# Optimization experiments

Hardware: AMD Instinct MI355X
Metric: run time of the kernel (lower is better)

Reference implementation:

```python
import jax, jax.numpy as jnp
import numpy as np

D_MODEL, D_STATE, D_CONV, D_INNER = 1024, 16, 4, 2048
BATCH, SEQ = 2, 2048


def setup_inputs() -> dict:
    key = jax.random.key(0)
    ks = jax.random.split(key, 12)
    s = 0.02
    inp = {
        "x": jax.random.normal(ks[0], (BATCH, SEQ, D_MODEL), jnp.float32),
        # Linear weights stored (in, out): y = x @ W + b (equivalent to torch x @ W.T + b)
        "W_in": jax.random.normal(ks[1], (D_MODEL, 2 * D_INNER), jnp.float32) * s,
        "b_in": jnp.zeros((2 * D_INNER,), jnp.float32),
        # depthwise conv kernel (OIH) with groups=d_inner -> (d_inner, 1, d_conv)
        "conv_w": jax.random.normal(ks[2], (D_INNER, 1, D_CONV), jnp.float32) * s,
        "conv_b": jnp.zeros((D_INNER,), jnp.float32),
        "W_x": jax.random.normal(ks[3], (D_INNER, 2 * D_STATE), jnp.float32) * s,
        "b_x": jnp.zeros((2 * D_STATE,), jnp.float32),
        "W_dt": jax.random.normal(ks[4], (D_INNER, D_INNER), jnp.float32) * s,
        "b_dt": jnp.zeros((D_INNER,), jnp.float32),
        # A_log init: log(arange(1..d_state)) tiled over d_inner, as in the module
        "A_log": jnp.log(jnp.tile(jnp.arange(1, D_STATE + 1, dtype=jnp.float32), (D_INNER, 1))),
        "D": jnp.ones((D_INNER,), jnp.float32),
        "W_out": jax.random.normal(ks[5], (D_INNER, D_MODEL), jnp.float32) * s,
        "b_out": jnp.zeros((D_MODEL,), jnp.float32),
    }
    return inp


def reference(x, W_in, b_in, conv_w, conv_b, W_x, b_x, W_dt, b_dt, A_log, D, W_out, b_out):
    d_inner, d_state = A_log.shape
    d_conv = conv_w.shape[-1]
    bsz, seq_len, _ = x.shape

    xz = x @ W_in + b_in                      # (B, L, 2*Din)
    xh, z = jnp.split(xz, 2, axis=-1)

    # causal depthwise conv: torch pads both sides by d_conv-1 then slices [:L]
    # == left-pad-only causal conv
    xc = jnp.transpose(xh, (0, 2, 1))         # (B, Din, L)
    xc = jax.lax.conv_general_dilated(
        xc, conv_w, window_strides=(1,), padding=[(d_conv - 1, 0)],
        dimension_numbers=("NCH", "OIH", "NCH"), feature_group_count=d_inner)
    xc = xc + conv_b[None, :, None]
    xh = jax.nn.silu(jnp.transpose(xc, (0, 2, 1)))  # (B, L, Din)

    A = -jnp.exp(A_log)                       # (Din, N)
    x_dbl = xh @ W_x + b_x                    # (B, L, 2N)
    Bmat = x_dbl[..., d_state:]               # second chunk; first chunk is discarded
    delta = jax.nn.softplus(xh @ W_dt + b_dt) # (B, L, Din)

    def step(h, inp):
        d_t, b_t, u_t = inp                    # (B,Din), (B,N), (B,Din)
        dA = jnp.exp(d_t[:, :, None] * A)      # (B, Din, N)
        dBu = d_t[:, :, None] * b_t[:, None, :] * u_t[:, :, None]
        h = dA * h + dBu
        return h, h.sum(-1)                    # y_t: (B, Din)

    h0 = jnp.zeros((bsz, d_inner, d_state), x.dtype)
    _, ys = jax.lax.scan(step, h0, (jnp.swapaxes(delta, 0, 1),
                                    jnp.swapaxes(Bmat, 0, 1),
                                    jnp.swapaxes(xh, 0, 1)))
    y = jnp.swapaxes(ys, 0, 1) + xh * D       # skip connection with D
    y = y * jax.nn.silu(z)                    # gate
    return y @ W_out + b_out                  # (B, L, d_model)
```

## Files before the change

kernel.cpp:

```cpp
#include <hip/hip_runtime.h>
#include <stdint.h>

#define NDM   1024
#define NDS   16
#define NDC   4
#define NDI   2048
#define NB    2
#define NL    2048
#define MROWS (NB*NL)
#define CCH   32
#define CLEN  64

typedef __bf16 bf16x8 __attribute__((ext_vector_type(8)));
typedef float  f32x4  __attribute__((ext_vector_type(4)));
typedef short  short8 __attribute__((ext_vector_type(8)));

__device__ __forceinline__ short f2bf(float f) {
  union { float f; unsigned u; } x; x.f = f;
  unsigned r = (x.u + 0x7FFFu + ((x.u >> 16) & 1u)) >> 16;
  return (short)r;
}

__device__ __forceinline__ size_t fgoff(int row, int k8, int K) {
  return (size_t)(row >> 4) * K * 16 + (size_t)k8 * 128 + (row & 15) * 8;
}

__global__ __launch_bounds__(256) void cvt_fg_kernel(
    const float* __restrict__ in, short* __restrict__ out) {
  __shared__ short slab[16][1032];
  const int tid = threadIdx.x;
  const int g = blockIdx.x;
  const float* p = in + (size_t)g * 16 * 1024;
  #pragma unroll
  for (int u = 0; u < 8; ++u) {
    int unit = u * 256 + tid;
    int rr = unit >> 7, cc = unit & 127;
    const float* rp = p + (size_t)rr * 1024 + cc * 8;
    #pragma unroll
    for (int e = 0; e < 8; ++e) slab[rr][cc * 8 + e] = f2bf(rp[e]);
  }
  __syncthreads();
  short* op = out + (size_t)g * 16384;
  #pragma unroll
  for (int u = 0; u < 8; ++u) {
    int u2 = u * 256 + tid;
    int rr = u2 & 15, k8 = u2 >> 4;
    *(short8*)&op[k8 * 128 + rr * 8] = *(short8*)&slab[rr][k8 * 8];
  }
}

__global__ __launch_bounds__(256) void transpose_fg_kernel(
    const float* __restrict__ in, short* __restrict__ out, int K, int N) {
  __shared__ float t[64][33];
  const int tx = threadIdx.x, ty = threadIdx.y;
  const int n0 = blockIdx.x * 32, k0 = blockIdx.y * 64;
  #pragma unroll
  for (int i = 0; i < 64; i += 8)
    t[ty + i][tx] = in[(size_t)(k0 + ty + i) * N + n0 + tx];
  __syncthreads();
  const int n = n0 + tx, k8 = (k0 >> 3) + ty;
  short8 v;
  #pragma unroll
  for (int e = 0; e < 8; ++e) v[e] = f2bf(t[ty * 8 + e][tx]);
  *(short8*)&out[fgoff(n, k8, K)] = v;
}

template<int BN, int EPI>
__global__ __launch_bounds__(256, 2) void gemm_fg_kernel(
    const short* __restrict__ A, const short* __restrict__ Bt,
    const float* __restrict__ bias, float* __restrict__ C,
    int M, int N, int K)
{
  const int tid  = threadIdx.x;
  const int lane = tid & 63;
  const int w    = tid >> 6;
  const int wM   = w >> 1;
  const int wN   = w & 1;
  const int g    = lane >> 4;
  const int r    = lane & 15;

  constexpr int FN = BN / 32;

  const int nx  = gridDim.x;
  const int nwg = nx * gridDim.y;
  const int bid = blockIdx.y * nx + blockIdx.x;
  const int swz = (bid & 7) * (nwg >> 3) + (bid >> 3);
  const int bm  = (swz / nx) * 128;
  const int bn  = (swz % nx) * BN;

  const short* pA[4];
  const short* pB[FN];
  #pragma unroll
  for (int m = 0; m < 4; ++m)
    pA[m] = A + (size_t)((bm >> 4) + wM * 4 + m) * K * 16 + lane * 8;
  #pragma unroll
  for (int n = 0; n < FN; ++n)
    pB[n] = Bt + (size_t)((bn >> 4) + wN * FN + n) * K * 16 + lane * 8;

  f32x4 acc[4][FN];
  #pragma unroll
  for (int m = 0; m < 4; ++m)
    #pragma unroll
    for (int n = 0; n < FN; ++n)
      acc[m][n] = (f32x4){0.f, 0.f, 0.f, 0.f};

  bf16x8 a0[4], b0[FN], a1[4], b1[FN];
  #pragma unroll
  for (int m = 0; m < 4; ++m) a0[m] = *(const bf16x8*)(pA[m]);
  #pragma unroll
  for (int n = 0; n < FN; ++n) b0[n] = *(const bf16x8*)(pB[n]);

  for (int kb = 0; kb < K; kb += 64) {
    if (kb + 32 < K) {
      #pragma unroll
      for (int m = 0; m < 4; ++m)
        a1[m] = *(const bf16x8*)(pA[m] + (size_t)(kb + 32) * 16);
      #pragma unroll
      for (int n = 0; n < FN; ++n)
        b1[n] = *(const bf16x8*)(pB[n] + (size_t)(kb + 32) * 16);
    }
    #pragma unroll
    for (int m = 0; m < 4; ++m)
      #pragma unroll
      for (int n = 0; n < FN; ++n)
        acc[m][n] = __builtin_amdgcn_mfma_f32_16x16x32_bf16(
            a0[m], b0[n], acc[m][n], 0, 0, 0);

    if (kb + 64 < K) {
      #pragma unroll
      for (int m = 0; m < 4; ++m)
        a0[m] = *(const bf16x8*)(pA[m] + (size_t)(kb + 64) * 16);
      #pragma unroll
      for (int n = 0; n < FN; ++n)
        b0[n] = *(const bf16x8*)(pB[n] + (size_t)(kb + 64) * 16);
    }
    #pragma unroll
    for (int m = 0; m < 4; ++m)
      #pragma unroll
      for (int n = 0; n < FN; ++n)
        acc[m][n] = __builtin_amdgcn_mfma_f32_16x16x32_bf16(
            a1[m], b1[n], acc[m][n], 0, 0, 0);
  }

  #pragma unroll
  for (int m = 0; m < 4; ++m) {
    const int row0 = bm + wM * 64 + m * 16 + g * 4;
    #pragma unroll
    for (int n = 0; n < FN; ++n) {
      const int col = bn + wN * (BN / 2) + n * 16 + r;
      const float bv = bias[col];
      #pragma unroll
      for (int e = 0; e < 4; ++e) {
        float v = acc[m][n][e] + bv;
        if (EPI == 1) v = (v > 15.f) ? v : log1pf(__expf(v));
        C[(size_t)(row0 + e) * N + col] = v;
      }
    }
  }
}

__global__ __launch_bounds__(256) void conv_silu_kernel(
    const float* __restrict__ xz, const float* __restrict__ cw,
    const float* __restrict__ cb, float* __restrict__ xh,
    short* __restrict__ xhbf) {
  __shared__ short slab[16][528];
  const int tid = threadIdx.x;
  const int c0 = blockIdx.x * 512;
  const int r0 = blockIdx.y * 16;
  const int b  = r0 >> 11;
  const int t0 = r0 & (NL - 1);
  const float* zbase = xz + ((size_t)b * NL) * (2 * NDI);

  #pragma unroll
  for (int u = 0; u < 4; ++u) {
    int unit = u * 256 + tid;
    int rr = unit >> 6, cc = unit & 63;
    int t = t0 + rr, c = c0 + cc * 8;
    float acc[8];
    #pragma unroll
    for (int e = 0; e < 8; ++e) acc[e] = cb[c + e];
    #pragma unroll
    for (int k = 0; k < NDC; ++k) {
      int tt = t - (NDC - 1) + k;
      if (tt >= 0) {
        const float* rp = zbase + (size_t)tt * (2 * NDI) + c;
        #pragma unroll
        for (int e = 0; e < 8; ++e) acc[e] += cw[(c + e) * NDC + k] * rp[e];
      }
    }
    float* xo = xh + (size_t)(r0 + rr) * NDI + c;
    #pragma unroll
    for (int e = 0; e < 8; ++e) {
      float s = acc[e] / (1.f + __expf(-acc[e]));
      xo[e] = s;
      slab[rr][cc * 8 + e] = f2bf(s);
    }
  }
  __syncthreads();
  short* op = xhbf + (size_t)(r0 >> 4) * NDI * 16 + (size_t)(c0 >> 3) * 128;
  #pragma unroll
  for (int u = 0; u < 4; ++u) {
    int u2 = u * 256 + tid;
    int rr = u2 & 15, q = u2 >> 4;
    *(short8*)&op[q * 128 + rr * 8] = *(short8*)&slab[rr][q * 8];
  }
}

__global__ __launch_bounds__(256) void bmat_kernel(
    const float* __restrict__ xh, const float* __restrict__ Wx,
    const float* __restrict__ bx, float* __restrict__ Bm) {
  const int row  = blockIdx.x * 4 + (threadIdx.x >> 6);
  const int lane = threadIdx.x & 63;
  const int s = lane & 15, q = lane >> 4;
  const float* xr = xh + (size_t)row * NDI;
  float acc = 0.f;
  for (int c = q * 512; c < (q + 1) * 512; ++c)
    acc += xr[c] * Wx[c * (2 * NDS) + NDS + s];
  acc += __shfl_xor(acc, 16);
  acc += __shfl_xor(acc, 32);
  if (lane < 16) Bm[(size_t)row * NDS + s] = acc + bx[NDS + s];
}

__device__ __forceinline__ size_t scoff(int b, int k, int c) {
  return (((size_t)b * CCH + k) * NDI + c) * NDS;
}

__global__ __launch_bounds__(256) void scan_p1_kernel(
    const float* __restrict__ delta, const float* __restrict__ Bm,
    const float* __restrict__ xh, const float* __restrict__ A_log,
    float* __restrict__ Pbuf, float* __restrict__ Hend) {
  const int i = blockIdx.x * 256 + threadIdx.x;
  const int c = i & (NDI - 1);
  const int k = (i >> 11) & (CCH - 1);
  const int b = i >> 16;
  const int t0 = k * CLEN;

  float Av[NDS];
  #pragma unroll
  for (int s = 0; s < NDS; ++s) Av[s] = -__expf(A_log[c * NDS + s]);

  const float* dp = delta + ((size_t)(b * NL + t0)) * NDI + c;
  const float* up = xh    + ((size_t)(b * NL + t0)) * NDI + c;
  const f32x4* Bp = (const f32x4*)(Bm + ((size_t)(b * NL + t0)) * NDS);

  float h[NDS], P[NDS];
  #pragma unroll
  for (int s = 0; s < NDS; ++s) { h[s] = 0.f; P[s] = 1.f; }

  #pragma unroll 4
  for (int j = 0; j < CLEN; ++j) {
    const float d = dp[(size_t)j * NDI];
    const float u = up[(size_t)j * NDI];
    f32x4 B0 = Bp[j * 4 + 0], B1 = Bp[j * 4 + 1];
    f32x4 B2 = Bp[j * 4 + 2], B3 = Bp[j * 4 + 3];
    const float du = d * u;
    float Bv[NDS];
    #pragma unroll
    for (int e = 0; e < 4; ++e) {
      Bv[e] = B0[e]; Bv[4 + e] = B1[e]; Bv[8 + e] = B2[e]; Bv[12 + e] = B3[e];
    }
    #pragma unroll
    for (int s = 0; s < NDS; ++s) {
      float dA = __expf(d * Av[s]);
      h[s] = dA * h[s] + du * Bv[s];
      P[s] *= dA;
    }
  }

  const size_t base = scoff(b, k, c);
  #pragma unroll
  for (int q = 0; q < 4; ++q) {
    *(f32x4*)&Pbuf[base + q * 4] = (f32x4){P[q*4], P[q*4+1], P[q*4+2], P[q*4+3]};
    *(f32x4*)&Hend[base + q * 4] = (f32x4){h[q*4], h[q*4+1], h[q*4+2], h[q*4+3]};
  }
}

__global__ __launch_bounds__(256) void scan_p2_kernel(
    const float* __restrict__ Pbuf, const float* __restrict__ Hend,
    float* __restrict__ Hin) {
  const int i = blockIdx.x * 256 + threadIdx.x;
  const int s = i & (NDS - 1);
  const int c = (i >> 4) & (NDI - 1);
  const int b = i >> 15;
  const size_t step = (size_t)NDI * NDS;
  const size_t base = scoff(b, 0, c) + s;
  float h = 0.f;
  #pragma unroll 8
  for (int k = 0; k < CCH; ++k) {
    Hin[base + (size_t)k * step] = h;
    h = Hend[base + (size_t)k * step] + Pbuf[base + (size_t)k * step] * h;
  }
}

__global__ __launch_bounds__(256) void scan_p3_kernel(
    const float* __restrict__ delta, const float* __restrict__ Bm,
    const float* __restrict__ xh, const float* __restrict__ A_log,
    const float* __restrict__ Hin, const float* __restrict__ Dvec,
    const float* __restrict__ xz, short* __restrict__ ybf) {
  const int tid = threadIdx.x;
  const int i = blockIdx.x * 256 + tid;
  const int c = i & (NDI - 1);
  const int k = (i >> 11) & (CCH - 1);
  const int b = i >> 16;
  const int t0 = k * CLEN;
  const int cb0 = (blockIdx.x * 256) & (NDI - 1);

  __shared__ float ylds[16][257];

  float Av[NDS];
  #pragma unroll
  for (int s = 0; s < NDS; ++s) Av[s] = -__expf(A_log[c * NDS + s]);
  const float dcoef = Dvec[c];

  const float* dp = delta + ((size_t)(b * NL + t0)) * NDI + c;
  const float* up = xh    + ((size_t)(b * NL + t0)) * NDI + c;
  const f32x4* Bp = (const f32x4*)(Bm + ((size_t)(b * NL + t0)) * NDS);
  const float* zp = xz    + ((size_t)(b * NL + t0)) * (2 * NDI) + NDI + c;

  const size_t base = scoff(b, k, c);
  float h[NDS];
  #pragma unroll
  for (int s = 0; s < NDS; ++s) h[s] = Hin[base + s];

  for (int j = 0; j < CLEN; ++j) {
    const float d = dp[(size_t)j * NDI];
    const float u = up[(size_t)j * NDI];
    f32x4 B0 = Bp[j * 4 + 0], B1 = Bp[j * 4 + 1];
    f32x4 B2 = Bp[j * 4 + 2], B3 = Bp[j * 4 + 3];
    const float du = d * u;
    float Bv[NDS];
    #pragma unroll
    for (int e = 0; e < 4; ++e) {
      Bv[e] = B0[e]; Bv[4 + e] = B1[e]; Bv[8 + e] = B2[e]; Bv[12 + e] = B3[e];
    }
    #pragma unroll
    for (int s = 0; s < NDS; ++s) {
      float dA = __expf(d * Av[s]);
      h[s] = dA * h[s] + du * Bv[s];
    }
    float sum01 = 0.f, sum23 = 0.f;
    #pragma unroll
    for (int s = 0; s < 8; ++s)  sum01 += h[s];
    #pragma unroll
    for (int s = 8; s < 16; ++s) sum23 += h[s];
    float y = sum01 + sum23 + u * dcoef;
    float z = zp[(size_t)j * (2 * NDI)];
    y *= z / (1.f + __expf(-z));
    ylds[j & 15][tid] = y;

    if ((j & 15) == 15) {
      __syncthreads();
      const int jb = j - 15;
      #pragma unroll
      for (int s2 = 0; s2 < 2; ++s2) {
        int u2 = tid + 256 * s2;
        int tt = u2 & 15, q = u2 >> 4;
        short8 v;
        #pragma unroll
        for (int e = 0; e < 8; ++e) v[e] = f2bf(ylds[tt][q * 8 + e]);
        int grow = b * NL + t0 + jb + tt;
        int k8 = (cb0 >> 3) + q;
        *(short8*)&ybf[fgoff(grow, k8, NDI)] = v;
      }
      __syncthreads();
    }
  }
}

extern "C" void kernel_launch(void* const* d_in, const int* in_sizes, int n_in,
                              void* d_out, int out_size, void* d_ws, size_t ws_size,
                              hipStream_t stream) {
  const float* x      = (const float*)d_in[0];
  const float* W_in   = (const float*)d_in[1];
  const float* b_in   = (const float*)d_in[2];
  const float* conv_w = (const float*)d_in[3];
  const float* conv_b = (const float*)d_in[4];
  const float* W_x    = (const float*)d_in[5];
  const float* b_x    = (const float*)d_in[6];
  const float* W_dt   = (const float*)d_in[7];
  const float* b_dt   = (const float*)d_in[8];
  const float* A_log  = (const float*)d_in[9];
  const float* Dv     = (const float*)d_in[10];
  const float* W_out  = (const float*)d_in[11];
  const float* b_out  = (const float*)d_in[12];
  float* out = (float*)d_out;

  char* w = (char*)d_ws;
  short* xbf   = (short*)(w);
  short* WtIn  = (short*)(w + 8388608);
  short* WtDt  = (short*)(w + 16777216);
  short* WtOut = (short*)(w + 25165824);
  float* xz    = (float*)(w + 29360128);
  float* xhf   = (float*)(w + 96468992);
  short* xhbf  = (short*)(w + 130023424);
  float* delta = (float*)(w + 146800640);
  float* Bm    = (float*)(w + 180355072);
  short* ybf   = (short*)(w + 214171648);
  float* Pbuf  = (float*)(w);
  float* Hend  = (float*)(w + 8388608);
  float* Hin   = (float*)(w + 16777216);

  cvt_fg_kernel<<<MROWS / 16, 256, 0, stream>>>(x, xbf);
  transpose_fg_kernel<<<dim3((2 * NDI) / 32, NDM / 64), dim3(32, 8), 0, stream>>>(
      W_in, WtIn, NDM, 2 * NDI);
  transpose_fg_kernel<<<dim3(NDI / 32, NDI / 64), dim3(32, 8), 0, stream>>>(
      W_dt, WtDt, NDI, NDI);
  transpose_fg_kernel<<<dim3(NDM / 32, NDI / 64), dim3(32, 8), 0, stream>>>(
      W_out, WtOut, NDI, NDM);

  gemm_fg_kernel<128, 0><<<dim3((2 * NDI) / 128, MROWS / 128), 256, 0, stream>>>(
      xbf, WtIn, b_in, xz, MROWS, 2 * NDI, NDM);

  conv_silu_kernel<<<dim3(NDI / 512, MROWS / 16), 256, 0, stream>>>(
      xz, conv_w, conv_b, xhf, xhbf);

  bmat_kernel<<<MROWS / 4, 256, 0, stream>>>(xhf, W_x, b_x, Bm);

  gemm_fg_kernel<128, 1><<<dim3(NDI / 128, MROWS / 128), 256, 0, stream>>>(
      xhbf, WtDt, b_dt, delta, MROWS, NDI, NDI);

  scan_p1_kernel<<<(NB * NDI * CCH) / 256, 256, 0, stream>>>(
      delta, Bm, xhf, A_log, Pbuf, Hend);
  scan_p2_kernel<<<(NB * NDI * NDS) / 256, 256, 0, stream>>>(Pbuf, Hend, Hin);
  scan_p3_kernel<<<(NB * NDI * CCH) / 256, 256, 0, stream>>>(
      delta, Bm, xhf, A_log, Hin, Dv, xz, ybf);

  gemm_fg_kernel<64, 0><<<dim3(NDM / 64, MROWS / 128), 256, 0, stream>>>(
      ybf, WtOut, b_out, out, MROWS, NDM, NDI);
}
```

Measured before the change: 347.9 us.

## Fuse B-projection into delta GEMM and store in_proj output as bf16

The W_x B-columns are appended to the transposed W_dt weight so the delta GEMM also computes Bmat in its epilogue, which removes the separate bmat_kernel. The in_proj GEMM now writes its output as bf16 through an LDS-staged coalesced store, which halves the bytes written and later read by the conv and scan kernels. The cost is extra tiles in the delta GEMM grid, reduced precision for z and conv inputs, and an added memset plus weight-conversion kernel.

```diff
diff --git a/kernel.cpp b/kernel.cpp
--- a/kernel.cpp
+++ b/kernel.cpp
@@ -20,6 +20,10 @@
   unsigned r = (x.u + 0x7FFFu + ((x.u >> 16) & 1u)) >> 16;
   return (short)r;
 }
+__device__ __forceinline__ float bf2f(short s) {
+  union { unsigned u; float f; } x; x.u = ((unsigned)(unsigned short)s) << 16;
+  return x.f;
+}
 
 __device__ __forceinline__ size_t fgoff(int row, int k8, int K) {
   return (size_t)(row >> 4) * K * 16 + (size_t)k8 * 128 + (row & 15) * 8;
@@ -65,11 +69,23 @@
   *(short8*)&out[fgoff(n, k8, K)] = v;
 }
 
+__global__ __launch_bounds__(256) void wx_fg_kernel(
+    const float* __restrict__ Wx, short* __restrict__ Wcat) {
+  int t = blockIdx.x * 256 + threadIdx.x;
+  int k8 = t >> 4, n = t & 15;
+  short8 v;
+  #pragma unroll
+  for (int e = 0; e < 8; ++e)
+    v[e] = f2bf(Wx[(size_t)(k8 * 8 + e) * (2 * NDS) + NDS + n]);
+  *(short8*)&Wcat[(size_t)128 * 2048 * 16 + (size_t)k8 * 128 + n * 8] = v;
+}
+
 template<int BN, int EPI>
 __global__ __launch_bounds__(256, 2) void gemm_fg_kernel(
     const short* __restrict__ A, const short* __restrict__ Bt,
     const float* __restrict__ bias, float* __restrict__ C,
-    int M, int N, int K)
+    short* __restrict__ Cb, float* __restrict__ Bm,
+    const float* __restrict__ bx, int M, int N, int K)
 {
   const int tid  = threadIdx.x;
   const int lane = tid & 63;
@@ -142,25 +158,57 @@
             a1[m], b1[n], acc[m][n], 0, 0, 0);
   }
 
-  #pragma unroll
-  for (int m = 0; m < 4; ++m) {
-    const int row0 = bm + wM * 64 + m * 16 + g * 4;
-    #pragma unroll
-    for (int n = 0; n < FN; ++n) {
-      const int col = bn + wN * (BN / 2) + n * 16 + r;
-      const float bv = bias[col];
-      #pragma unroll
-      for (int e = 0; e < 4; ++e) {
-        float v = acc[m][n][e] + bv;
-        if (EPI == 1) v = (v > 15.f) ? v : log1pf(__expf(v));
-        C[(size_t)(row0 + e) * N + col] = v;
+  if constexpr (EPI == 2) {
+    __shared__ short ctile[128][136];
+    #pragma unroll
+    for (int m = 0; m < 4; ++m) {
+      const int rl0 = wM * 64 + m * 16 + g * 4;
+      #pragma unroll
+      for (int n = 0; n < FN; ++n) {
+        const int cl = wN * (BN / 2) + n * 16 + r;
+        const float bv = bias[bn + cl];
+        #pragma unroll
+        for (int e = 0; e < 4; ++e)
+          ctile[rl0 + e][cl] = f2bf(acc[m][n][e] + bv);
       }
     }
+    __syncthreads();
+    #pragma unroll
+    for (int it = 0; it < (128 * BN / 8) / 256; ++it) {
+      int id = it * 256 + tid;
+      int rowL = id / (BN / 8), c8 = id % (BN / 8);
+      *(short8*)&Cb[(size_t)(bm + rowL) * N + bn + c8 * 8] =
+          *(short8*)&ctile[rowL][c8 * 8];
+    }
+  } else {
+    #pragma unroll
+    for (int m = 0; m < 4; ++m) {
+      const int row0 = bm + wM * 64 + m * 16 + g * 4;
+      #pragma unroll
+      for (int n = 0; n < FN; ++n) {
+        const int colbase = bn + wN * (BN / 2) + n * 16;
+        const int col = colbase + r;
+        if (EPI == 0 || colbase < 2048) {
+          const float bv = bias[col];
+          #pragma unroll
+          for (int e = 0; e < 4; ++e) {
+            float v = acc[m][n][e] + bv;
+            if (EPI == 1) v = (v > 15.f) ? v : log1pf(__expf(v));
+            C[(size_t)(row0 + e) * N + col] = v;
+          }
+        } else if (EPI == 1 && colbase < 2064) {
+          const float bv = bx[NDS + r];
+          #pragma unroll
+          for (int e = 0; e < 4; ++e)
+            Bm[(size_t)(row0 + e) * NDS + r] = acc[m][n][e] + bv;
+        }
+      }
+    }
   }
 }
 
 __global__ __launch_bounds__(256) void conv_silu_kernel(
-    const float* __restrict__ xz, const float* __restrict__ cw,
+    const short* __restrict__ xz, const float* __restrict__ cw,
     const float* __restrict__ cb, float* __restrict__ xh,
     short* __restrict__ xhbf) {
   __shared__ short slab[16][528];
@@ -169,7 +217,7 @@
   const int r0 = blockIdx.y * 16;
   const int b  = r0 >> 11;
   const int t0 = r0 & (NL - 1);
-  const float* zbase = xz + ((size_t)b * NL) * (2 * NDI);
+  const short* zbase = xz + ((size_t)b * NL) * (2 * NDI);
 
   #pragma unroll
   for (int u = 0; u < 4; ++u) {
@@ -183,9 +231,10 @@
     for (int k = 0; k < NDC; ++k) {
       int tt = t - (NDC - 1) + k;
       if (tt >= 0) {
-        const float* rp = zbase + (size_t)tt * (2 * NDI) + c;
+        short8 rv = *(const short8*)(zbase + (size_t)tt * (2 * NDI) + c);
         #pragma unroll
-        for (int e = 0; e < 8; ++e) acc[e] += cw[(c + e) * NDC + k] * rp[e];
+        for (int e = 0; e < 8; ++e)
+          acc[e] += cw[(c + e) * NDC + k] * bf2f(rv[e]);
       }
     }
     float* xo = xh + (size_t)(r0 + rr) * NDI + c;
@@ -204,21 +253,6 @@
     int rr = u2 & 15, q = u2 >> 4;
     *(short8*)&op[q * 128 + rr * 8] = *(short8*)&slab[rr][q * 8];
   }
-}
-
-__global__ __launch_bounds__(256) void bmat_kernel(
-    const float* __restrict__ xh, const float* __restrict__ Wx,
-    const float* __restrict__ bx, float* __restrict__ Bm) {
-  const int row  = blockIdx.x * 4 + (threadIdx.x >> 6);
-  const int lane = threadIdx.x & 63;
-  const int s = lane & 15, q = lane >> 4;
-  const float* xr = xh + (size_t)row * NDI;
-  float acc = 0.f;
-  for (int c = q * 512; c < (q + 1) * 512; ++c)
-    acc += xr[c] * Wx[c * (2 * NDS) + NDS + s];
-  acc += __shfl_xor(acc, 16);
-  acc += __shfl_xor(acc, 32);
-  if (lane < 16) Bm[(size_t)row * NDS + s] = acc + bx[NDS + s];
 }
 
 __device__ __forceinline__ size_t scoff(int b, int k, int c) {
@@ -296,7 +330,7 @@
     const float* __restrict__ delta, const float* __restrict__ Bm,
     const float* __restrict__ xh, const float* __restrict__ A_log,
     const float* __restrict__ Hin, const float* __restrict__ Dvec,
-    const float* __restrict__ xz, short* __restrict__ ybf) {
+    const short* __restrict__ xz, short* __restrict__ ybf) {
   const int tid = threadIdx.x;
   const int i = blockIdx.x * 256 + tid;
   const int c = i & (NDI - 1);
@@ -315,7 +349,7 @@
   const float* dp = delta + ((size_t)(b * NL + t0)) * NDI + c;
   const float* up = xh    + ((size_t)(b * NL + t0)) * NDI + c;
   const f32x4* Bp = (const f32x4*)(Bm + ((size_t)(b * NL + t0)) * NDS);
-  const float* zp = xz    + ((size_t)(b * NL + t0)) * (2 * NDI) + NDI + c;
+  const short* zp = xz    + ((size_t)(b * NL + t0)) * (2 * NDI) + NDI + c;
 
   const size_t base = scoff(b, k, c);
   float h[NDS];
@@ -344,7 +378,7 @@
     #pragma unroll
     for (int s = 8; s < 16; ++s) sum23 += h[s];
     float y = sum01 + sum23 + u * dcoef;
-    float z = zp[(size_t)j * (2 * NDI)];
+    float z = bf2f(zp[(size_t)j * (2 * NDI)]);
     y *= z / (1.f + __expf(-z));
     ylds[j & 15][tid] = y;
 
@@ -388,43 +422,47 @@
   char* w = (char*)d_ws;
   short* xbf   = (short*)(w);
   short* WtIn  = (short*)(w + 8388608);
-  short* WtDt  = (short*)(w + 16777216);
-  short* WtOut = (short*)(w + 25165824);
-  float* xz    = (float*)(w + 29360128);
-  float* xhf   = (float*)(w + 96468992);
-  short* xhbf  = (short*)(w + 130023424);
-  float* delta = (float*)(w + 146800640);
-  float* Bm    = (float*)(w + 180355072);
-  short* ybf   = (short*)(w + 214171648);
+  short* WtCat = (short*)(w + 16777216);
+  short* WtOut = (short*)(w + 25690112);
+  short* xzbf  = (short*)(w + 29884416);
+  float* xhf   = (float*)(w + 63438848);
+  short* xhbf  = (short*)(w + 96993280);
+  float* delta = (float*)(w + 113770496);
+  float* Bm    = (float*)(w + 147324928);
+  short* ybf   = (short*)(w + 147587072);
   float* Pbuf  = (float*)(w);
   float* Hend  = (float*)(w + 8388608);
   float* Hin   = (float*)(w + 16777216);
+
+  hipMemsetAsync((char*)WtCat + (size_t)129 * 65536, 0, 7 * 65536, stream);
 
   cvt_fg_kernel<<<MROWS / 16, 256, 0, stream>>>(x, xbf);
   transpose_fg_kernel<<<dim3((2 * NDI) / 32, NDM / 64), dim3(32, 8), 0, stream>>>(
       W_in, WtIn, NDM, 2 * NDI);
   transpose_fg_kernel<<<dim3(NDI / 32, NDI / 64), dim3(32, 8), 0, stream>>>(
-      W_dt, WtDt, NDI, NDI);
+      W_dt, WtCat, NDI, NDI);
+  wx_fg_kernel<<<16, 256, 0, stream>>>(W_x, WtCat);
   transpose_fg_kernel<<<dim3(NDM / 32, NDI / 64), dim3(32, 8), 0, stream>>>(
       W_out, WtOut, NDI, NDM);
 
-  gemm_fg_kernel<128, 0><<<dim3((2 * NDI) / 128, MROWS / 128), 256, 0, stream>>>(
-      xbf, WtIn, b_in, xz, MROWS, 2 * NDI, NDM);
+  gemm_fg_kernel<128, 2><<<dim3((2 * NDI) / 128, MROWS / 128), 256, 0, stream>>>(
+      xbf, WtIn, b_in, nullptr, xzbf, nullptr, nullptr,
+      MROWS, 2 * NDI, NDM);
 
   conv_silu_kernel<<<dim3(NDI / 512, MROWS / 16), 256, 0, stream>>>(
-      xz, conv_w, conv_b, xhf, xhbf);
-
-  bmat_kernel<<<MROWS / 4, 256, 0, stream>>>(xhf, W_x, b_x, Bm);
-
-  gemm_fg_kernel<128, 1><<<dim3(NDI / 128, MROWS / 128), 256, 0, stream>>>(
-      xhbf, WtDt, b_dt, delta, MROWS, NDI, NDI);
+      xzbf, conv_w, conv_b, xhf, xhbf);
+
+  gemm_fg_kernel<128, 1><<<dim3(2176 / 128, MROWS / 128), 256, 0, stream>>>(
+      xhbf, WtCat, b_dt, delta, nullptr, Bm, b_x,
+      MROWS, NDI, NDI);
 
   scan_p1_kernel<<<(NB * NDI * CCH) / 256, 256, 0, stream>>>(
       delta, Bm, xhf, A_log, Pbuf, Hend);
   scan_p2_kernel<<<(NB * NDI * NDS) / 256, 256, 0, stream>>>(Pbuf, Hend, Hin);
   scan_p3_kernel<<<(NB * NDI * CCH) / 256, 256, 0, stream>>>(
-      delta, Bm, xhf, A_log, Hin, Dv, xz, ybf);
+      delta, Bm, xhf, A_log, Hin, Dv, xzbf, ybf);
 
   gemm_fg_kernel<64, 0><<<dim3(NDM / 64, MROWS / 128), 256, 0, stream>>>(
-      ybf, WtOut, b_out, out, MROWS, NDM, NDI);
-}
+      ybf, WtOut, b_out, out, nullptr, nullptr, nullptr,
+      MROWS, NDM, NDI);
+}
```

Measured after the change: 327.4 us. -5.9%, faster.
